# Optimization experiments

Hardware: AMD Instinct MI355X
Metric: run time of the kernel (lower is better)

## Reference

```python
import jax, jax.numpy as jnp
import numpy as np

NEG = -1000000.0

def setup_inputs() -> dict:
    key = jax.random.key(0)
    k1, k2, k3, k4, k5 = jax.random.split(key, 5)
    B, Lq, Lm, Din, Dout = 8, 2048, 2048, 1024, 1024
    query = jax.random.normal(k1, (B, Lq, Din), dtype=jnp.float32)
    memories = jax.random.normal(k2, (B, Lm, Dout), dtype=jnp.float32)
    mask = jax.random.randint(k3, (B, Lq, Lm), 0, 2, dtype=jnp.int32)
    # Linear(in_features=1024, out_features=1024)
    bound = 1.0 / np.sqrt(Din)
    W = jax.random.uniform(k4, (Dout, Din), minval=-bound, maxval=bound, dtype=jnp.float32)
    b = jax.random.uniform(k5, (Dout,), minval=-bound, maxval=bound, dtype=jnp.float32)
    return {"query": query, "memories": memories, "mask": mask, "W": W, "b": b}

def reference(query, memories, mask, W, b):
    # projected query: [B, Lq, Dout]
    q = jnp.einsum('bqi,oi->bqo', query, W) + b
    # additive binary mask: 1 -> 0, 0 -> -1e6
    add_mask = (1.0 - mask.astype(q.dtype)) * NEG
    # unscaled Luong scores: [B, Lq, Lm]
    logits = jnp.einsum('bqd,bmd->bqm', q, memories) + add_mask
    weights = jax.nn.softmax(logits, axis=-1)
    out = jnp.einsum('bqm,bmd->bqd', weights, memories)
    return out
```

## Files before the change

### kernel.cpp

```cpp
#include <hip/hip_runtime.h>

typedef float    f32x4 __attribute__((ext_vector_type(4)));
typedef _Float16 f16x4 __attribute__((ext_vector_type(4)));
typedef _Float16 f16x8 __attribute__((ext_vector_type(8)));

__device__ __forceinline__ void gload16(const void* g, void* l) {
  __builtin_amdgcn_global_load_lds(
      (const __attribute__((address_space(1))) void*)g,
      (__attribute__((address_space(3))) void*)l, 16, 0, 0);
}

#define MFMA16(d, a, b) __builtin_amdgcn_mfma_f32_16x16x32_f16(a, b, d, 0, 0, 0)

template <bool STG>
__device__ __forceinline__ void ktile256(
    char* L, int d, size_t go,
    const char* aSrc0, const char* aSrc1,
    const char* bSrc0, const char* bSrc1,
    int ldsStage, int wr, int wc, int l15, int rcb,
    f32x4 (&acc)[8][4]) {
  const char* Ab0 = L + d * 32768;
  const char* Bb0 = L + 65536 + d * 32768;
  const int dn = d ^ 1;
  f16x8 af[4], bf[4];

  #pragma unroll
  for (int m = 0; m < 4; m++)
    af[m] = *(const f16x8*)(Ab0 + (wr + m * 16 + l15) * 64 + rcb);
  #pragma unroll
  for (int n = 0; n < 4; n++)
    bf[n] = *(const f16x8*)(Bb0 + (wc + n * 16 + l15) * 64 + rcb);
  if constexpr (STG) {
    char* dst = L + dn * 32768 + ldsStage;
    gload16(aSrc0 + go, dst);
    gload16(aSrc1 + go, dst + 1024);
  }
  __builtin_amdgcn_s_barrier();
  __builtin_amdgcn_s_setprio(1);
  #pragma unroll
  for (int m = 0; m < 4; m++)
    #pragma unroll
    for (int n = 0; n < 4; n++)
      acc[m][n] = MFMA16(acc[m][n], af[m], bf[n]);
  __builtin_amdgcn_s_setprio(0);
  __builtin_amdgcn_s_barrier();

  #pragma unroll
  for (int m = 0; m < 4; m++)
    af[m] = *(const f16x8*)(Ab0 + (wr + (4 + m) * 16 + l15) * 64 + rcb);
  if constexpr (STG) {
    char* dst = L + 65536 + dn * 32768 + ldsStage;
    gload16(bSrc0 + go, dst);
    gload16(bSrc1 + go, dst + 1024);
    asm volatile("s_waitcnt vmcnt(4)" ::: "memory");
  } else {
    asm volatile("s_waitcnt vmcnt(0)" ::: "memory");
  }
  __builtin_amdgcn_s_barrier();
  __builtin_amdgcn_s_setprio(1);
  #pragma unroll
  for (int m = 0; m < 4; m++)
    #pragma unroll
    for (int n = 0; n < 4; n++)
      acc[4 + m][n] = MFMA16(acc[4 + m][n], af[m], bf[n]);
  __builtin_amdgcn_s_setprio(0);
  __builtin_amdgcn_s_barrier();

  #pragma unroll
  for (int m = 0; m < 4; m++)
    af[m] = *(const f16x8*)(Ab0 + 16384 + (wr + m * 16 + l15) * 64 + rcb);
  #pragma unroll
  for (int n = 0; n < 4; n++)
    bf[n] = *(const f16x8*)(Bb0 + 16384 + (wc + n * 16 + l15) * 64 + rcb);
  if constexpr (STG) {
    char* dst = L + dn * 32768 + 16384 + ldsStage;
    gload16(aSrc0 + go + 64, dst);
    gload16(aSrc1 + go + 64, dst + 1024);
  }
  __builtin_amdgcn_s_barrier();
  __builtin_amdgcn_s_setprio(1);
  #pragma unroll
  for (int m = 0; m < 4; m++)
    #pragma unroll
    for (int n = 0; n < 4; n++)
      acc[m][n] = MFMA16(acc[m][n], af[m], bf[n]);
  __builtin_amdgcn_s_setprio(0);
  __builtin_amdgcn_s_barrier();

  #pragma unroll
  for (int m = 0; m < 4; m++)
    af[m] = *(const f16x8*)(Ab0 + 16384 + (wr + (4 + m) * 16 + l15) * 64 + rcb);
  if constexpr (STG) {
    char* dst = L + 65536 + dn * 32768 + 16384 + ldsStage;
    gload16(bSrc0 + go + 64, dst);
    gload16(bSrc1 + go + 64, dst + 1024);
    asm volatile("s_waitcnt vmcnt(4)" ::: "memory");
  }
  __builtin_amdgcn_s_barrier();
  __builtin_amdgcn_s_setprio(1);
  #pragma unroll
  for (int m = 0; m < 4; m++)
    #pragma unroll
    for (int n = 0; n < 4; n++)
      acc[4 + m][n] = MFMA16(acc[4 + m][n], af[m], bf[n]);
  __builtin_amdgcn_s_setprio(0);
  __builtin_amdgcn_s_barrier();
}

template <typename TOUT, bool BIAS>
__global__ __launch_bounds__(512) void gemm256(
    const _Float16* __restrict__ A, const _Float16* __restrict__ B,
    const float* __restrict__ bias, TOUT* __restrict__ Cp,
    int M, int N, int K, long sA, long sB, long sC) {
  __shared__ _Float16 lds[65536];
  char* const L = (char*)lds;
  const int tid = threadIdx.x;
  const int w = tid >> 6, l = tid & 63;
  const int l15 = l & 15, q = l >> 4;
  const int wr = (w >> 2) * 128, wc = (w & 3) * 64;
  const int m0 = blockIdx.y * 256, n0 = blockIdx.x * 256;
  const _Float16* Ab = A + (size_t)blockIdx.z * sA;
  const _Float16* Bb = B + (size_t)blockIdx.z * sB;

  const int scb = (((l & 3) ^ ((l >> 3) & 3)) << 4);
  const int sr0 = w * 32 + (l >> 2);
  const char* aSrc0 = (const char*)(Ab + (size_t)(m0 + sr0) * K) + scb;
  const char* aSrc1 = (const char*)(Ab + (size_t)(m0 + sr0 + 16) * K) + scb;
  const char* bSrc0 = (const char*)(Bb + (size_t)(n0 + sr0) * K) + scb;
  const char* bSrc1 = (const char*)(Bb + (size_t)(n0 + sr0 + 16) * K) + scb;
  const int ldsStage = w * 2048;
  const int rcb = ((q ^ ((l15 >> 1) & 3)) << 4);

  f32x4 acc[8][4] = {};
  const int NT = K >> 6;

  {
    char* dA = L + ldsStage;
    char* dB = L + 65536 + ldsStage;
    gload16(aSrc0, dA);       gload16(aSrc1, dA + 1024);
    gload16(bSrc0, dB);       gload16(bSrc1, dB + 1024);
    gload16(aSrc0 + 64, dA + 16384); gload16(aSrc1 + 64, dA + 16384 + 1024);
    gload16(bSrc0 + 64, dB + 16384); gload16(bSrc1 + 64, dB + 16384 + 1024);
    asm volatile("s_waitcnt vmcnt(4)" ::: "memory");
  }
  __builtin_amdgcn_s_barrier();

  for (int t = 0; t < NT - 1; ++t)
    ktile256<true>(L, t & 1, (size_t)(t + 1) * 128, aSrc0, aSrc1, bSrc0, bSrc1,
                   ldsStage, wr, wc, l15, rcb, acc);
  ktile256<false>(L, (NT - 1) & 1, 0, aSrc0, aSrc1, bSrc0, bSrc1,
                  ldsStage, wr, wc, l15, rcb, acc);

  TOUT* C = Cp + (size_t)blockIdx.z * sC;
  const int q4 = q * 4;
  #pragma unroll
  for (int n = 0; n < 4; n++) {
    int col = n0 + wc + n * 16 + l15;
    float bb = BIAS ? bias[col] : 0.0f;
    #pragma unroll
    for (int m = 0; m < 8; m++) {
      int rowb = m0 + wr + m * 16 + q4;
      #pragma unroll
      for (int rr = 0; rr < 4; rr++)
        C[(size_t)(rowb + rr) * N + col] = (TOUT)(acc[m][n][rr] + bb);
    }
  }
}

__global__ __launch_bounds__(256) void transpose16_kernel(
    const _Float16* __restrict__ src, _Float16* __restrict__ dst) {
  const int Lm = 2048, D = 1024;
  __shared__ _Float16 tile[64 * 64];
  const int d0 = blockIdx.x * 64, m0 = blockIdx.y * 64;
  const _Float16* s = src + (size_t)blockIdx.z * Lm * D;
  _Float16*       d = dst + (size_t)blockIdx.z * D * Lm;
  const int tid = threadIdx.x;
  #pragma unroll
  for (int it = 0; it < 2; it++) {
    int idx = tid + it * 256;
    int mm = idx >> 3, g = idx & 7;
    int pg = g ^ ((mm >> 3) & 7);
    *(f16x8*)&tile[mm * 64 + pg * 8] =
        *(const f16x8*)&s[(size_t)(m0 + mm) * D + d0 + g * 8];
  }
  __syncthreads();
  #pragma unroll
  for (int it = 0; it < 2; it++) {
    int idx = tid + it * 256;
    int dd = idx >> 3, mc = (idx & 7) * 8;
    f16x8 h;
    #pragma unroll
    for (int j = 0; j < 8; j++) {
      int row = mc + j;
      int pg = (dd >> 3) ^ ((row >> 3) & 7);
      h[j] = tile[row * 64 + pg * 8 + (dd & 7)];
    }
    *(f16x8*)&d[(size_t)(d0 + dd) * Lm + m0 + mc] = h;
  }
}

__global__ __launch_bounds__(256) void softmax_kernel(
    const int* __restrict__ mask, _Float16* __restrict__ wbuf) {
  const int Lm = 2048;
  size_t row = blockIdx.x;
  _Float16* wr = wbuf + row * Lm;
  const int* mr = mask + row * Lm;
  int tid = threadIdx.x;
  f16x8 lv = *(const f16x8*)&wr[tid * 8];
  int4 ma = *(const int4*)&mr[tid * 8];
  int4 mb = *(const int4*)&mr[tid * 8 + 4];
  int mk[8] = {ma.x, ma.y, ma.z, ma.w, mb.x, mb.y, mb.z, mb.w};
  float v[8];
  float mx = -3.0e38f;
  #pragma unroll
  for (int i = 0; i < 8; i++) {
    float l = (float)lv[i];
    if (mk[i] == 0) l += -1000000.0f;
    v[i] = l;
    mx = fmaxf(mx, l);
  }
  #pragma unroll
  for (int off = 32; off > 0; off >>= 1) mx = fmaxf(mx, __shfl_down(mx, off, 64));
  __shared__ float red[4];
  int wv = tid >> 6;
  if ((tid & 63) == 0) red[wv] = mx;
  __syncthreads();
  mx = fmaxf(fmaxf(red[0], red[1]), fmaxf(red[2], red[3]));
  __syncthreads();
  float s = 0.f;
  #pragma unroll
  for (int i = 0; i < 8; i++) { v[i] = __expf(v[i] - mx); s += v[i]; }
  #pragma unroll
  for (int off = 32; off > 0; off >>= 1) s += __shfl_down(s, off, 64);
  if ((tid & 63) == 0) red[wv] = s;
  __syncthreads();
  float inv = 1.0f / (red[0] + red[1] + red[2] + red[3]);
  f16x8 o;
  #pragma unroll
  for (int i = 0; i < 8; i++) o[i] = (_Float16)(v[i] * inv);
  *(f16x8*)&wr[tid * 8] = o;
}

__global__ __launch_bounds__(256) void cvt8_kernel(const float* __restrict__ x,
                                                   _Float16* __restrict__ y) {
  size_t i = (size_t)(blockIdx.x * 256 + threadIdx.x) * 8;
  f32x4 a = *(const f32x4*)&x[i];
  f32x4 b = *(const f32x4*)&x[i + 4];
  f16x8 h = {(_Float16)a[0], (_Float16)a[1], (_Float16)a[2], (_Float16)a[3],
             (_Float16)b[0], (_Float16)b[1], (_Float16)b[2], (_Float16)b[3]};
  *(f16x8*)&y[i] = h;
}

extern "C" void kernel_launch(void* const* d_in, const int* in_sizes, int n_in,
                              void* d_out, int out_size, void* d_ws, size_t ws_size,
                              hipStream_t stream) {
  const float* query = (const float*)d_in[0];
  const float* mem   = (const float*)d_in[1];
  const int*   mask  = (const int*)d_in[2];
  const float* W     = (const float*)d_in[3];
  const float* bias  = (const float*)d_in[4];
  float* out = (float*)d_out;

  char* ws = (char*)d_ws;
  _Float16* qproj  = (_Float16*)ws;
  _Float16* memT   = (_Float16*)ws;
  _Float16* queryh = (_Float16*)(ws + (size_t)32 * 1024 * 1024);
  _Float16* Wh     = (_Float16*)(ws + (size_t)64 * 1024 * 1024);
  _Float16* wbuf   = (_Float16*)(ws + (size_t)32 * 1024 * 1024);
  _Float16* memh   = (_Float16*)d_out;

  const long LQK = 2048L * 1024, LQM = 2048L * 2048;

  cvt8_kernel<<<dim3(512),  256, 0, stream>>>(W, Wh);
  cvt8_kernel<<<dim3(8192), 256, 0, stream>>>(query, queryh);
  cvt8_kernel<<<dim3(8192), 256, 0, stream>>>(mem, memh);
  gemm256<_Float16, true><<<dim3(4, 64, 1), 512, 0, stream>>>(
      queryh, Wh, bias, qproj, 16384, 1024, 1024, 0, 0, 0);
  gemm256<_Float16, false><<<dim3(8, 8, 8), 512, 0, stream>>>(
      qproj, memh, nullptr, wbuf, 2048, 2048, 1024, LQK, LQK, LQM);
  softmax_kernel<<<dim3(16384), 256, 0, stream>>>(mask, wbuf);
  transpose16_kernel<<<dim3(16, 32, 8), 256, 0, stream>>>(memh, memT);
  gemm256<float, false><<<dim3(4, 8, 8), 512, 0, stream>>>(
      wbuf, memT, nullptr, out, 2048, 1024, 2048, LQM, LQK, LQK);
}
```

Measured before the change: 508.8 us.

## Issue next-tile loads upfront and cut per-k-tile barriers to one

Each 64-wide k-tile now issues all eight global-to-LDS loads for the next stage at its start. It then runs four MFMA phases, interleaving LDS fragment reads with MFMA using two sets of A/B registers, with no barriers in between. A single vmcnt(0) wait and barrier at the end of the tile replace the eight barriers and staggered vmcnt(4) waits used before. This removes most of the wave synchronization stalls per tile, at the cost of higher register pressure. Global latency must now be hidden within one tile's compute.

Result: no change. 502.9 us (-1.1%).

```diff
diff --git a/kernel.cpp b/kernel.cpp
--- a/kernel.cpp
+++ b/kernel.cpp
@@ -22,89 +22,79 @@
   const char* Ab0 = L + d * 32768;
   const char* Bb0 = L + 65536 + d * 32768;
   const int dn = d ^ 1;
-  f16x8 af[4], bf[4];
-
-  #pragma unroll
-  for (int m = 0; m < 4; m++)
-    af[m] = *(const f16x8*)(Ab0 + (wr + m * 16 + l15) * 64 + rcb);
+
+  if constexpr (STG) {
+    char* dA = L + dn * 32768 + ldsStage;
+    char* dB = L + 65536 + dn * 32768 + ldsStage;
+    gload16(aSrc0 + go, dA);
+    gload16(aSrc1 + go, dA + 1024);
+    gload16(aSrc0 + go + 64, dA + 16384);
+    gload16(aSrc1 + go + 64, dA + 16384 + 1024);
+    gload16(bSrc0 + go, dB);
+    gload16(bSrc1 + go, dB + 1024);
+    gload16(bSrc0 + go + 64, dB + 16384);
+    gload16(bSrc1 + go + 64, dB + 16384 + 1024);
+  }
+
+  f16x8 afX[4], afY[4], bfX[4], bfY[4];
+
+  #pragma unroll
+  for (int m = 0; m < 4; m++)
+    afX[m] = *(const f16x8*)(Ab0 + (wr + m * 16 + l15) * 64 + rcb);
   #pragma unroll
   for (int n = 0; n < 4; n++)
-    bf[n] = *(const f16x8*)(Bb0 + (wc + n * 16 + l15) * 64 + rcb);
+    bfX[n] = *(const f16x8*)(Bb0 + (wc + n * 16 + l15) * 64 + rcb);
+  #pragma unroll
+  for (int m = 0; m < 4; m++)
+    afY[m] = *(const f16x8*)(Ab0 + (wr + (4 + m) * 16 + l15) * 64 + rcb);
+
+  __builtin_amdgcn_s_setprio(1);
+  #pragma unroll
+  for (int m = 0; m < 4; m++)
+    #pragma unroll
+    for (int n = 0; n < 4; n++)
+      acc[m][n] = MFMA16(acc[m][n], afX[m], bfX[n]);
+  __builtin_amdgcn_s_setprio(0);
+
+  #pragma unroll
+  for (int n = 0; n < 4; n++)
+    bfY[n] = *(const f16x8*)(Bb0 + 16384 + (wc + n * 16 + l15) * 64 + rcb);
+  #pragma unroll
+  for (int m = 0; m < 4; m++)
+    afX[m] = *(const f16x8*)(Ab0 + 16384 + (wr + m * 16 + l15) * 64 + rcb);
+
+  __builtin_amdgcn_s_setprio(1);
+  #pragma unroll
+  for (int m = 0; m < 4; m++)
+    #pragma unroll
+    for (int n = 0; n < 4; n++)
+      acc[4 + m][n] = MFMA16(acc[4 + m][n], afY[m], bfX[n]);
+  __builtin_amdgcn_s_setprio(0);
+
+  #pragma unroll
+  for (int m = 0; m < 4; m++)
+    afY[m] = *(const f16x8*)(Ab0 + 16384 + (wr + (4 + m) * 16 + l15) * 64 + rcb);
+
+  __builtin_amdgcn_s_setprio(1);
+  #pragma unroll
+  for (int m = 0; m < 4; m++)
+    #pragma unroll
+    for (int n = 0; n < 4; n++)
+      acc[m][n] = MFMA16(acc[m][n], afX[m], bfY[n]);
+  __builtin_amdgcn_s_setprio(0);
+
+  __builtin_amdgcn_s_setprio(1);
+  #pragma unroll
+  for (int m = 0; m < 4; m++)
+    #pragma unroll
+    for (int n = 0; n < 4; n++)
+      acc[4 + m][n] = MFMA16(acc[4 + m][n], afY[m], bfY[n]);
+  __builtin_amdgcn_s_setprio(0);
+
   if constexpr (STG) {
-    char* dst = L + dn * 32768 + ldsStage;
-    gload16(aSrc0 + go, dst);
-    gload16(aSrc1 + go, dst + 1024);
-  }
-  __builtin_amdgcn_s_barrier();
-  __builtin_amdgcn_s_setprio(1);
-  #pragma unroll
-  for (int m = 0; m < 4; m++)
-    #pragma unroll
-    for (int n = 0; n < 4; n++)
-      acc[m][n] = MFMA16(acc[m][n], af[m], bf[n]);
-  __builtin_amdgcn_s_setprio(0);
-  __builtin_amdgcn_s_barrier();
-
-  #pragma unroll
-  for (int m = 0; m < 4; m++)
-    af[m] = *(const f16x8*)(Ab0 + (wr + (4 + m) * 16 + l15) * 64 + rcb);
-  if constexpr (STG) {
-    char* dst = L + 65536 + dn * 32768 + ldsStage;
-    gload16(bSrc0 + go, dst);
-    gload16(bSrc1 + go, dst + 1024);
-    asm volatile("s_waitcnt vmcnt(4)" ::: "memory");
-  } else {
     asm volatile("s_waitcnt vmcnt(0)" ::: "memory");
-  }
-  __builtin_amdgcn_s_barrier();
-  __builtin_amdgcn_s_setprio(1);
-  #pragma unroll
-  for (int m = 0; m < 4; m++)
-    #pragma unroll
-    for (int n = 0; n < 4; n++)
-      acc[4 + m][n] = MFMA16(acc[4 + m][n], af[m], bf[n]);
-  __builtin_amdgcn_s_setprio(0);
-  __builtin_amdgcn_s_barrier();
-
-  #pragma unroll
-  for (int m = 0; m < 4; m++)
-    af[m] = *(const f16x8*)(Ab0 + 16384 + (wr + m * 16 + l15) * 64 + rcb);
-  #pragma unroll
-  for (int n = 0; n < 4; n++)
-    bf[n] = *(const f16x8*)(Bb0 + 16384 + (wc + n * 16 + l15) * 64 + rcb);
-  if constexpr (STG) {
-    char* dst = L + dn * 32768 + 16384 + ldsStage;
-    gload16(aSrc0 + go + 64, dst);
-    gload16(aSrc1 + go + 64, dst + 1024);
-  }
-  __builtin_amdgcn_s_barrier();
-  __builtin_amdgcn_s_setprio(1);
-  #pragma unroll
-  for (int m = 0; m < 4; m++)
-    #pragma unroll
-    for (int n = 0; n < 4; n++)
-      acc[m][n] = MFMA16(acc[m][n], af[m], bf[n]);
-  __builtin_amdgcn_s_setprio(0);
-  __builtin_amdgcn_s_barrier();
-
-  #pragma unroll
-  for (int m = 0; m < 4; m++)
-    af[m] = *(const f16x8*)(Ab0 + 16384 + (wr + (4 + m) * 16 + l15) * 64 + rcb);
-  if constexpr (STG) {
-    char* dst = L + 65536 + dn * 32768 + 16384 + ldsStage;
-    gload16(bSrc0 + go + 64, dst);
-    gload16(bSrc1 + go + 64, dst + 1024);
-    asm volatile("s_waitcnt vmcnt(4)" ::: "memory");
-  }
-  __builtin_amdgcn_s_barrier();
-  __builtin_amdgcn_s_setprio(1);
-  #pragma unroll
-  for (int m = 0; m < 4; m++)
-    #pragma unroll
-    for (int n = 0; n < 4; n++)
-      acc[4 + m][n] = MFMA16(acc[4 + m][n], af[m], bf[n]);
-  __builtin_amdgcn_s_setprio(0);
-  __builtin_amdgcn_s_barrier();
+    __builtin_amdgcn_s_barrier();
+  }
 }
 
 template <typename TOUT, bool BIAS>
@@ -138,10 +128,10 @@
     char* dA = L + ldsStage;
     char* dB = L + 65536 + ldsStage;
     gload16(aSrc0, dA);       gload16(aSrc1, dA + 1024);
+    gload16(aSrc0 + 64, dA + 16384); gload16(aSrc1 + 64, dA + 16384 + 1024);
     gload16(bSrc0, dB);       gload16(bSrc1, dB + 1024);
-    gload16(aSrc0 + 64, dA + 16384); gload16(aSrc1 + 64, dA + 16384 + 1024);
     gload16(bSrc0 + 64, dB + 16384); gload16(bSrc1 + 64, dB + 16384 + 1024);
-    asm volatile("s_waitcnt vmcnt(4)" ::: "memory");
+    asm volatile("s_waitcnt vmcnt(0)" ::: "memory");
   }
   __builtin_amdgcn_s_barrier();
 
```
